# Kernel optimization log

Hardware: AMD Instinct MI355X
Metric: run time of the kernel (lower is better)

The kernel has to match this reference:

```python
import jax, jax.numpy as jnp
import numpy as np

NUM_HEADS = 12
EMBED_DIM = 768


def setup_inputs() -> dict:
    key = jax.random.key(0)
    ks = jax.random.split(key, 7)
    B, N, E = 4, 2048, EMBED_DIM
    s = 1.0 / np.sqrt(E)  # init scale to keep activations sane
    return {
        "x": jax.random.normal(ks[0], (B, N, E), dtype=jnp.float32),
        "Wq": jax.random.normal(ks[1], (E, E), dtype=jnp.float32) * s,
        "bq": jnp.zeros((E,), dtype=jnp.float32),
        "Wk": jax.random.normal(ks[2], (E, E), dtype=jnp.float32) * s,
        "bk": jnp.zeros((E,), dtype=jnp.float32),
        "Wv": jax.random.normal(ks[3], (E, E), dtype=jnp.float32) * s,
        "bv": jnp.zeros((E,), dtype=jnp.float32),
    }


def reference(x, Wq, bq, Wk, bk, Wv, bv):
    B, N, E = x.shape
    H = NUM_HEADS
    d = E // H
    # QKV projections, split into heads: b n (h d) -> b h n d
    q = (x @ Wq + bq).reshape(B, N, H, d).transpose(0, 2, 1, 3)
    k = (x @ Wk + bk).reshape(B, N, H, d).transpose(0, 2, 1, 3)
    v = (x @ Wv + bv).reshape(B, N, H, d).transpose(0, 2, 1, 3)
    # NOTE: non-standard scale = 1/sqrt(num_heads), not 1/sqrt(head_dim)
    scale = 1.0 / jnp.sqrt(jnp.asarray(H, dtype=x.dtype))
    attn_weight = jnp.einsum("bhqd,bhkd->bhqk", q, k) * scale
    # NOTE: softmax over the QUERY axis (dim=2), not the key axis
    attn_score = jax.nn.softmax(attn_weight, axis=2)
    out = jnp.einsum("bhqk,bhkd->bhqd", attn_score, v)
    # b h n d -> b n (h d)
    return out.transpose(0, 2, 1, 3).reshape(B, N, E)
```

## Files before the change

### kernel.cpp

```cpp
#include <hip/hip_runtime.h>

#define NN 2048
#define EE 768
#define HH 12
#define DD 64
#define BHX 48
#define MM 8192

typedef unsigned short u16;
typedef unsigned int u32;
typedef __attribute__((ext_vector_type(8))) short bf16x8;
typedef __attribute__((ext_vector_type(4))) float f32x4;

#if __has_builtin(__builtin_amdgcn_exp2f)
#define EX2(x) __builtin_amdgcn_exp2f(x)
#else
#define EX2(x) exp2f(x)
#endif

#define MFMA16(a, b, c) __builtin_amdgcn_mfma_f32_16x16x32_bf16((a), (b), (c), 0, 0, 0)

__device__ __forceinline__ u16 f2bf(float f) {
    u32 u = __builtin_bit_cast(u32, f);
    u32 r = (u + 0x7FFFu + ((u >> 16) & 1u)) >> 16;
    return (u16)r;
}
__device__ __forceinline__ float bf2f(u16 b) {
    u32 u = ((u32)b) << 16;
    return __builtin_bit_cast(float, u);
}
__device__ __forceinline__ void gload_lds16(const u16* g, u16* l) {
    __builtin_amdgcn_global_load_lds((const __attribute__((address_space(1))) void*)g,
                                     (__attribute__((address_space(3))) void*)l, 16, 0, 0);
}

__global__ __launch_bounds__(256) void k_cvt_x(const float* __restrict__ x, u16* __restrict__ xb, int n8) {
    int i = blockIdx.x * 256 + threadIdx.x;
    if (i >= n8) return;
    const float4* x4 = (const float4*)x;
    float4 a = x4[i * 2], b = x4[i * 2 + 1];
    uint4 o;
    o.x = (u32)f2bf(a.x) | ((u32)f2bf(a.y) << 16);
    o.y = (u32)f2bf(a.z) | ((u32)f2bf(a.w) << 16);
    o.z = (u32)f2bf(b.x) | ((u32)f2bf(b.y) << 16);
    o.w = (u32)f2bf(b.z) | ((u32)f2bf(b.w) << 16);
    ((uint4*)xb)[i] = o;
}

__global__ __launch_bounds__(256) void k_wt(const float* __restrict__ Wq, const float* __restrict__ Wk,
                                            const float* __restrict__ Wv, u16* __restrict__ wt) {
    int idx = blockIdx.x * 256 + threadIdx.x;
    int wsel = idx / (EE * EE);
    int rem = idx - wsel * (EE * EE);
    int j = rem / EE;
    int k = rem - j * EE;
    const float* W = (wsel == 0) ? Wq : (wsel == 1 ? Wk : Wv);
    wt[(size_t)wsel * EE * EE + (size_t)j * EE + k] = f2bf(W[(size_t)k * EE + j]);
}

__global__ __launch_bounds__(256) void k_proj(const u16* __restrict__ xb, const u16* __restrict__ wt,
                                              const float* __restrict__ bq, const float* __restrict__ bk,
                                              const float* __restrict__ bv, u16* __restrict__ qh,
                                              u16* __restrict__ kh, u16* __restrict__ vh) {
    __shared__ u16 lA[128 * 32];
    __shared__ u16 lB[128 * 32];
    const int z = blockIdx.z;
    const u16* Wz = wt + (size_t)z * EE * EE;
    const float* bias = (z == 0) ? bq : (z == 1 ? bk : bv);
    u16* outp = (z == 0) ? qh : (z == 1 ? kh : vh);
    const float oscale = (z == 0) ? (0.28867513459481287f * 1.4426950408889634f) : 1.0f;
    const int tid = threadIdx.x;
    const int lane = tid & 63, w = tid >> 6;
    const int wr = w >> 1, wc = w & 1, lr = lane & 15, lg = lane >> 4;
    const int m0 = blockIdx.x * 128, n0 = blockIdx.y * 128;

    f32x4 acc[4][4];
#pragma unroll
    for (int mi = 0; mi < 4; mi++)
#pragma unroll
        for (int ni = 0; ni < 4; ni++) acc[mi][ni] = (f32x4){0.f, 0.f, 0.f, 0.f};

    for (int kt = 0; kt < EE; kt += 32) {
#pragma unroll
        for (int i = 0; i < 2; i++) {
            int c = i * 256 + tid;
            int row = c >> 2, cc = c & 3;
            gload_lds16(xb + (size_t)(m0 + row) * EE + kt + cc * 8, &lA[c * 8]);
            gload_lds16(Wz + (size_t)(n0 + row) * EE + kt + cc * 8, &lB[c * 8]);
        }
        __syncthreads();
        bf16x8 af[4], bfr[4];
#pragma unroll
        for (int mi = 0; mi < 4; mi++) af[mi] = *(const bf16x8*)&lA[(wr * 64 + mi * 16 + lr) * 32 + lg * 8];
#pragma unroll
        for (int ni = 0; ni < 4; ni++) bfr[ni] = *(const bf16x8*)&lB[(wc * 64 + ni * 16 + lr) * 32 + lg * 8];
#pragma unroll
        for (int mi = 0; mi < 4; mi++)
#pragma unroll
            for (int ni = 0; ni < 4; ni++) acc[mi][ni] = MFMA16(af[mi], bfr[ni], acc[mi][ni]);
        __syncthreads();
    }

#pragma unroll
    for (int ni = 0; ni < 4; ni++) {
        int col = n0 + wc * 64 + ni * 16 + lr;
        float bb = bias[col];
        int h = col >> 6, dd = col & 63;
#pragma unroll
        for (int mi = 0; mi < 4; mi++) {
            int rowbase = m0 + wr * 64 + mi * 16 + lg * 4;
#pragma unroll
            for (int r = 0; r < 4; r++) {
                int row = rowbase + r;
                int b = row >> 11, nn = row & 2047;
                outp[(((size_t)b * HH + h) * NN + nn) * DD + dd] = f2bf((acc[mi][ni][r] + bb) * oscale);
            }
        }
    }
}

__global__ __launch_bounds__(256) void k_stats(const u16* __restrict__ qh, const u16* __restrict__ kh,
                                               float* __restrict__ rlb) {
    __shared__ u16 lds[2][4096];
    const int lin = blockIdx.x;
    const int nb = (lin & 7) * 96 + (lin >> 3);
    const int bh = nb >> 4, kb = nb & 15;
    const int tid = threadIdx.x, lane = tid & 63, w = tid >> 6;
    const int lr = lane & 15, lg = lane >> 4;
    const int kw0 = kb * 128 + w * 32;
    const u16* Q = qh + (size_t)bh * NN * DD;
    const u16* K = kh + (size_t)bh * NN * DD;

    bf16x8 kf[2][2];
#pragma unroll
    for (int t = 0; t < 2; t++)
#pragma unroll
        for (int kk = 0; kk < 2; kk++)
            kf[t][kk] = *(const bf16x8*)(K + (size_t)(kw0 + t * 16 + lr) * DD + kk * 32 + lg * 8);

    const u16* qp[2];
#pragma unroll
    for (int i = 0; i < 2; i++) {
        int c = tid + i * 256;
        int f = c >> 6;
        int qrow = (f >> 1) * 16 + (c & 15);
        int doff = (f & 1) * 32 + ((c >> 4) & 3) * 8;
        qp[i] = Q + (size_t)qrow * DD + doff;
    }

#define STAGE_Q(buf, q0)                                              \
    do {                                                              \
        _Pragma("unroll") for (int i = 0; i < 2; i++) {               \
            int c = tid + i * 256;                                    \
            gload_lds16(qp[i] + (size_t)(q0) * DD, &lds[buf][c * 8]); \
        }                                                             \
    } while (0)

    STAGE_Q(0, 0);
    __syncthreads();
    float lacc[2] = {0.f, 0.f};
    int cur = 0;
    for (int it = 0; it < 32; ++it) {
        if (it < 31) STAGE_Q(cur ^ 1, (it + 1) * 64);
#pragma unroll
        for (int qt = 0; qt < 4; ++qt) {
            bf16x8 qa0 = *(const bf16x8*)&lds[cur][(qt * 2 + 0) * 512 + lane * 8];
            bf16x8 qa1 = *(const bf16x8*)&lds[cur][(qt * 2 + 1) * 512 + lane * 8];
#pragma unroll
            for (int t = 0; t < 2; t++) {
                f32x4 s = (f32x4){0.f, 0.f, 0.f, 0.f};
                s = MFMA16(qa0, kf[t][0], s);
                s = MFMA16(qa1, kf[t][1], s);
                lacc[t] += EX2(s[0]) + EX2(s[1]) + EX2(s[2]) + EX2(s[3]);
            }
        }
        __syncthreads();
        cur ^= 1;
    }
#undef STAGE_Q
#pragma unroll
    for (int t = 0; t < 2; t++) {
        float v = lacc[t];
        v += __shfl_xor(v, 16);
        v += __shfl_xor(v, 32);
        if (lane < 16) rlb[(size_t)bh * NN + kw0 + t * 16 + lane] = 1.0f / v;
    }
}

__global__ __launch_bounds__(256) void k_vtrans(const u16* __restrict__ vh, const float* __restrict__ rlb,
                                                u16* __restrict__ vt) {
    __shared__ u16 lds[64 * 80];
    const int bh = blockIdx.x, n0 = blockIdx.y * 64;
    const int tid = threadIdx.x;
    const u16* src = vh + (size_t)bh * NN * DD + (size_t)n0 * DD;
    const float* rlp = rlb + (size_t)bh * NN + n0;
#pragma unroll
    for (int i = 0; i < 2; i++) {
        int c = i * 256 + tid;
        int row = c >> 3, dc = c & 7;
        uint4 vraw = *(const uint4*)(src + row * DD + dc * 8);
        float rk = rlp[row];
        u32 uu[4] = {vraw.x, vraw.y, vraw.z, vraw.w};
#pragma unroll
        for (int j = 0; j < 4; j++) {
            u16 e0 = (u16)(uu[j] & 0xffff), e1 = (u16)(uu[j] >> 16);
            lds[(dc * 8 + 2 * j) * 80 + row] = f2bf(rk * bf2f(e0));
            lds[(dc * 8 + 2 * j + 1) * 80 + row] = f2bf(rk * bf2f(e1));
        }
    }
    __syncthreads();
    u16* dst = vt + (size_t)bh * DD * NN + n0;
#pragma unroll
    for (int i = 0; i < 2; i++) {
        int c = i * 256 + tid;
        int d = c >> 3, nc = c & 7;
        int w0 = nc * 8;
        uint2 a = *(const uint2*)&lds[d * 80 + w0];
        uint2 b = *(const uint2*)&lds[d * 80 + w0 + 4];
        int hi32 = (w0 >> 5) * 32;
        int wa = w0 & 31, wb = (w0 + 4) & 31;
        int ca = ((wa & 15) >> 2) * 8 + (wa >> 4) * 4;
        int cb = ((wb & 15) >> 2) * 8 + (wb >> 4) * 4;
        *(uint2*)(dst + (size_t)d * NN + hi32 + ca) = a;
        *(uint2*)(dst + (size_t)d * NN + hi32 + cb) = b;
    }
}

__global__ __launch_bounds__(256) void k_attn(const u16* __restrict__ qh, const u16* __restrict__ kh,
                                              const u16* __restrict__ vt, float* __restrict__ out) {
    __shared__ u16 lds[2][8192];
    const int lin = blockIdx.x;
    const int nb = (lin & 7) * 96 + (lin >> 3);
    const int bh = nb >> 4, qb = nb & 15;
    const int tid = threadIdx.x, lane = tid & 63, w = tid >> 6;
    const int lr = lane & 15, lg = lane >> 4;
    const int qw0 = qb * 128 + w * 32;
    const u16* Q = qh + (size_t)bh * NN * DD;
    const u16* K = kh + (size_t)bh * NN * DD;
    const u16* V = vt + (size_t)bh * DD * NN;

    bf16x8 qf[2][2];
#pragma unroll
    for (int mi = 0; mi < 2; mi++)
#pragma unroll
        for (int kk = 0; kk < 2; kk++)
            qf[mi][kk] = *(const bf16x8*)(Q + (size_t)(qw0 + mi * 16 + lr) * DD + kk * 32 + lg * 8);

    const u16* kp[2];
    const u16* vp[2];
#pragma unroll
    for (int i = 0; i < 2; i++) {
        int c = tid + i * 256;
        int f = c >> 6;
        int rk = (f >> 2) * 32 + ((f >> 1) & 1) * 16 + (c & 15);
        int doff = (f & 1) * 32 + ((c >> 4) & 3) * 8;
        kp[i] = K + (size_t)rk * DD + doff;
        int drow = (f & 3) * 16 + (c & 15);
        int koff = (f >> 2) * 32 + ((c >> 4) & 3) * 8;
        vp[i] = V + (size_t)drow * NN + koff;
    }

#define STAGE_KV(buf, k0)                                                  \
    do {                                                                   \
        _Pragma("unroll") for (int i = 0; i < 2; i++) {                    \
            int c = tid + i * 256;                                         \
            gload_lds16(kp[i] + (size_t)(k0) * DD, &lds[buf][c * 8]);      \
            gload_lds16(vp[i] + (size_t)(k0), &lds[buf][4096 + c * 8]);    \
        }                                                                  \
    } while (0)

    f32x4 acc[2][4];
#pragma unroll
    for (int mi = 0; mi < 2; mi++)
#pragma unroll
        for (int di = 0; di < 4; di++) acc[mi][di] = (f32x4){0.f, 0.f, 0.f, 0.f};

    STAGE_KV(0, 0);
    __syncthreads();
    int cur = 0;
    for (int it = 0; it < 32; ++it) {
        if (it < 31) STAGE_KV(cur ^ 1, (it + 1) * 64);
        const u16* Lk = &lds[cur][0];
        const u16* Lv = &lds[cur][4096];
#pragma unroll
        for (int kc = 0; kc < 2; ++kc) {
            bf16x8 kf2[2][2];
#pragma unroll
            for (int t = 0; t < 2; t++)
#pragma unroll
                for (int kk = 0; kk < 2; kk++)
                    kf2[t][kk] = *(const bf16x8*)&Lk[((kc * 2 + t) * 2 + kk) * 512 + lane * 8];
            bf16x8 vf[4];
#pragma unroll
            for (int di = 0; di < 4; di++)
                vf[di] = *(const bf16x8*)&Lv[(kc * 4 + di) * 512 + lane * 8];
#pragma unroll
            for (int mi = 0; mi < 2; mi++) {
                f32x4 s0 = (f32x4){0.f, 0.f, 0.f, 0.f}, s1 = (f32x4){0.f, 0.f, 0.f, 0.f};
                s0 = MFMA16(kf2[0][0], qf[mi][0], s0);
                s0 = MFMA16(kf2[0][1], qf[mi][1], s0);
                s1 = MFMA16(kf2[1][0], qf[mi][0], s1);
                s1 = MFMA16(kf2[1][1], qf[mi][1], s1);
                uint4 pu;
                pu.x = (u32)f2bf(EX2(s0[0])) | ((u32)f2bf(EX2(s0[1])) << 16);
                pu.y = (u32)f2bf(EX2(s0[2])) | ((u32)f2bf(EX2(s0[3])) << 16);
                pu.z = (u32)f2bf(EX2(s1[0])) | ((u32)f2bf(EX2(s1[1])) << 16);
                pu.w = (u32)f2bf(EX2(s1[2])) | ((u32)f2bf(EX2(s1[3])) << 16);
                bf16x8 pa = __builtin_bit_cast(bf16x8, pu);
#pragma unroll
                for (int di = 0; di < 4; di++) acc[mi][di] = MFMA16(pa, vf[di], acc[mi][di]);
            }
        }
        __syncthreads();
        cur ^= 1;
    }
#undef STAGE_KV

    const int b = bh / HH, h = bh % HH;
#pragma unroll
    for (int mi = 0; mi < 2; mi++)
#pragma unroll
        for (int di = 0; di < 4; di++)
#pragma unroll
            for (int r = 0; r < 4; r++) {
                int q = qw0 + mi * 16 + lg * 4 + r;
                int d = di * 16 + lr;
                out[((size_t)(b * NN + q)) * EE + h * DD + d] = acc[mi][di][r];
            }
}

extern "C" void kernel_launch(void* const* d_in, const int* in_sizes, int n_in,
                              void* d_out, int out_size, void* d_ws, size_t ws_size,
                              hipStream_t stream) {
    const float* x = (const float*)d_in[0];
    const float* Wq = (const float*)d_in[1];
    const float* bq = (const float*)d_in[2];
    const float* Wk = (const float*)d_in[3];
    const float* bk = (const float*)d_in[4];
    const float* Wv = (const float*)d_in[5];
    const float* bv = (const float*)d_in[6];
    float* out = (float*)d_out;
    char* ws = (char*)d_ws;

    size_t off = 0;
    u16* xb = (u16*)(ws + off); off += (size_t)MM * EE * 2;
    u16* wt = (u16*)(ws + off); off += (size_t)3 * EE * EE * 2;
    u16* qh = (u16*)(ws + off); off += (size_t)BHX * NN * DD * 2;
    u16* kh = (u16*)(ws + off); off += (size_t)BHX * NN * DD * 2;
    u16* vh = (u16*)(ws + off); off += (size_t)BHX * NN * DD * 2;
    u16* vt = (u16*)(ws + off); off += (size_t)BHX * NN * DD * 2;
    float* rlb = (float*)(ws + off); off += (size_t)BHX * NN * 4;

    k_cvt_x<<<dim3(3072), dim3(256), 0, stream>>>(x, xb, MM * EE / 8);
    k_wt<<<dim3(6912), dim3(256), 0, stream>>>(Wq, Wk, Wv, wt);
    k_proj<<<dim3(64, 6, 3), dim3(256), 0, stream>>>(xb, wt, bq, bk, bv, qh, kh, vh);
    k_stats<<<dim3(768), dim3(256), 0, stream>>>(qh, kh, rlb);
    k_vtrans<<<dim3(48, 32), dim3(256), 0, stream>>>(vh, rlb, vt);
    k_attn<<<dim3(768), dim3(256), 0, stream>>>(qh, kh, vt, out);
}
```

Baseline: 190.2 us.

## Split attention block across 8 waves with 16 query rows each

```diff
diff --git a/kernel.cpp b/kernel.cpp
--- a/kernel.cpp
+++ b/kernel.cpp
@@ -226,7 +226,7 @@
     }
 }
 
-__global__ __launch_bounds__(256) void k_attn(const u16* __restrict__ qh, const u16* __restrict__ kh,
+__global__ __launch_bounds__(512) void k_attn(const u16* __restrict__ qh, const u16* __restrict__ kh,
                                               const u16* __restrict__ vt, float* __restrict__ out) {
     __shared__ u16 lds[2][8192];
     const int lin = blockIdx.x;
@@ -234,46 +234,34 @@
     const int bh = nb >> 4, qb = nb & 15;
     const int tid = threadIdx.x, lane = tid & 63, w = tid >> 6;
     const int lr = lane & 15, lg = lane >> 4;
-    const int qw0 = qb * 128 + w * 32;
+    const int qw0 = qb * 128 + w * 16;
     const u16* Q = qh + (size_t)bh * NN * DD;
     const u16* K = kh + (size_t)bh * NN * DD;
     const u16* V = vt + (size_t)bh * DD * NN;
 
-    bf16x8 qf[2][2];
-#pragma unroll
-    for (int mi = 0; mi < 2; mi++)
-#pragma unroll
-        for (int kk = 0; kk < 2; kk++)
-            qf[mi][kk] = *(const bf16x8*)(Q + (size_t)(qw0 + mi * 16 + lr) * DD + kk * 32 + lg * 8);
-
-    const u16* kp[2];
-    const u16* vp[2];
-#pragma unroll
-    for (int i = 0; i < 2; i++) {
-        int c = tid + i * 256;
-        int f = c >> 6;
-        int rk = (f >> 2) * 32 + ((f >> 1) & 1) * 16 + (c & 15);
-        int doff = (f & 1) * 32 + ((c >> 4) & 3) * 8;
-        kp[i] = K + (size_t)rk * DD + doff;
-        int drow = (f & 3) * 16 + (c & 15);
-        int koff = (f >> 2) * 32 + ((c >> 4) & 3) * 8;
-        vp[i] = V + (size_t)drow * NN + koff;
-    }
-
-#define STAGE_KV(buf, k0)                                                  \
-    do {                                                                   \
-        _Pragma("unroll") for (int i = 0; i < 2; i++) {                    \
-            int c = tid + i * 256;                                         \
-            gload_lds16(kp[i] + (size_t)(k0) * DD, &lds[buf][c * 8]);      \
-            gload_lds16(vp[i] + (size_t)(k0), &lds[buf][4096 + c * 8]);    \
-        }                                                                  \
+    bf16x8 qf[2];
+#pragma unroll
+    for (int kk = 0; kk < 2; kk++)
+        qf[kk] = *(const bf16x8*)(Q + (size_t)(qw0 + lr) * DD + kk * 32 + lg * 8);
+
+    const int c = tid;
+    const int f = c >> 6;
+    const int rk = (f >> 2) * 32 + ((f >> 1) & 1) * 16 + (c & 15);
+    const int doff = (f & 1) * 32 + ((c >> 4) & 3) * 8;
+    const u16* kp = K + (size_t)rk * DD + doff;
+    const int drow = (f & 3) * 16 + (c & 15);
+    const int koff = (f >> 2) * 32 + ((c >> 4) & 3) * 8;
+    const u16* vp = V + (size_t)drow * NN + koff;
+
+#define STAGE_KV(buf, k0)                                          \
+    do {                                                           \
+        gload_lds16(kp + (size_t)(k0) * DD, &lds[buf][c * 8]);     \
+        gload_lds16(vp + (size_t)(k0), &lds[buf][4096 + c * 8]);   \
     } while (0)
 
-    f32x4 acc[2][4];
-#pragma unroll
-    for (int mi = 0; mi < 2; mi++)
-#pragma unroll
-        for (int di = 0; di < 4; di++) acc[mi][di] = (f32x4){0.f, 0.f, 0.f, 0.f};
+    f32x4 acc[4];
+#pragma unroll
+    for (int di = 0; di < 4; di++) acc[di] = (f32x4){0.f, 0.f, 0.f, 0.f};
 
     STAGE_KV(0, 0);
     __syncthreads();
@@ -294,22 +282,19 @@
 #pragma unroll
             for (int di = 0; di < 4; di++)
                 vf[di] = *(const bf16x8*)&Lv[(kc * 4 + di) * 512 + lane * 8];
-#pragma unroll
-            for (int mi = 0; mi < 2; mi++) {
-                f32x4 s0 = (f32x4){0.f, 0.f, 0.f, 0.f}, s1 = (f32x4){0.f, 0.f, 0.f, 0.f};
-                s0 = MFMA16(kf2[0][0], qf[mi][0], s0);
-                s0 = MFMA16(kf2[0][1], qf[mi][1], s0);
-                s1 = MFMA16(kf2[1][0], qf[mi][0], s1);
-                s1 = MFMA16(kf2[1][1], qf[mi][1], s1);
-                uint4 pu;
-                pu.x = (u32)f2bf(EX2(s0[0])) | ((u32)f2bf(EX2(s0[1])) << 16);
-                pu.y = (u32)f2bf(EX2(s0[2])) | ((u32)f2bf(EX2(s0[3])) << 16);
-                pu.z = (u32)f2bf(EX2(s1[0])) | ((u32)f2bf(EX2(s1[1])) << 16);
-                pu.w = (u32)f2bf(EX2(s1[2])) | ((u32)f2bf(EX2(s1[3])) << 16);
-                bf16x8 pa = __builtin_bit_cast(bf16x8, pu);
-#pragma unroll
-                for (int di = 0; di < 4; di++) acc[mi][di] = MFMA16(pa, vf[di], acc[mi][di]);
-            }
+            f32x4 s0 = (f32x4){0.f, 0.f, 0.f, 0.f}, s1 = (f32x4){0.f, 0.f, 0.f, 0.f};
+            s0 = MFMA16(kf2[0][0], qf[0], s0);
+            s0 = MFMA16(kf2[0][1], qf[1], s0);
+            s1 = MFMA16(kf2[1][0], qf[0], s1);
+            s1 = MFMA16(kf2[1][1], qf[1], s1);
+            uint4 pu;
+            pu.x = (u32)f2bf(EX2(s0[0])) | ((u32)f2bf(EX2(s0[1])) << 16);
+            pu.y = (u32)f2bf(EX2(s0[2])) | ((u32)f2bf(EX2(s0[3])) << 16);
+            pu.z = (u32)f2bf(EX2(s1[0])) | ((u32)f2bf(EX2(s1[1])) << 16);
+            pu.w = (u32)f2bf(EX2(s1[2])) | ((u32)f2bf(EX2(s1[3])) << 16);
+            bf16x8 pa = __builtin_bit_cast(bf16x8, pu);
+#pragma unroll
+            for (int di = 0; di < 4; di++) acc[di] = MFMA16(pa, vf[di], acc[di]);
         }
         __syncthreads();
         cur ^= 1;
@@ -318,15 +303,13 @@
 
     const int b = bh / HH, h = bh % HH;
 #pragma unroll
-    for (int mi = 0; mi < 2; mi++)
-#pragma unroll
-        for (int di = 0; di < 4; di++)
-#pragma unroll
-            for (int r = 0; r < 4; r++) {
-                int q = qw0 + mi * 16 + lg * 4 + r;
-                int d = di * 16 + lr;
-                out[((size_t)(b * NN + q)) * EE + h * DD + d] = acc[mi][di][r];
-            }
+    for (int di = 0; di < 4; di++)
+#pragma unroll
+        for (int r = 0; r < 4; r++) {
+            int q = qw0 + lg * 4 + r;
+            int d = di * 16 + lr;
+            out[((size_t)(b * NN + q)) * EE + h * DD + d] = acc[di][r];
+        }
 }
 
 extern "C" void kernel_launch(void* const* d_in, const int* in_sizes, int n_in,
@@ -356,5 +339,5 @@
     k_proj<<<dim3(64, 6, 3), dim3(256), 0, stream>>>(xb, wt, bq, bk, bv, qh, kh, vh);
     k_stats<<<dim3(768), dim3(256), 0, stream>>>(qh, kh, rlb);
     k_vtrans<<<dim3(48, 32), dim3(256), 0, stream>>>(vh, rlb, vt);
-    k_attn<<<dim3(768), dim3(256), 0, stream>>>(qh, kh, vt, out);
-}
+    k_attn<<<dim3(768), dim3(512), 0, stream>>>(qh, kh, vt, out);
+}
```

After: 185.0 us. 2.7% less time.
